# Optimization experiments

Measured on AMD Instinct MI355X. Metric: run time of the kernel, lower is better.

## Reference

```python
import jax, jax.numpy as jnp
import numpy as np

SOFTMAX_TEMP = 0.01
WINDOW_SIZE = 2
B_TOTAL, C, N = 8, 256, 512
H = W = 256


def _l2_normalize(x, axis):
    # F.normalize: x / max(||x||, eps)
    n = jnp.sqrt(jnp.sum(x * x, axis=axis, keepdims=True))
    return x / jnp.maximum(n, 1e-12)


def _bilinear_sample(img, coords):
    """Bilinear sample img [b,c,H,W] at pixel coords [b,n,2] (u=x, v=y),
    align_corners=True semantics (coords are direct pixel positions)."""
    b, c, h, w = img.shape
    u = jnp.clip(coords[..., 0], 0.0, w - 1.0)
    v = jnp.clip(coords[..., 1], 0.0, h - 1.0)
    u0 = jnp.floor(u); v0 = jnp.floor(v)
    u1 = jnp.minimum(u0 + 1.0, w - 1.0)
    v1 = jnp.minimum(v0 + 1.0, h - 1.0)
    wu = u - u0; wv = v - v0
    flat = img.reshape(b, c, h * w)
    n = coords.shape[1]
    def gather(vi, ui):
        idx = (vi * w + ui).astype(jnp.int32)  # [b,n]
        return jnp.take_along_axis(flat, jnp.broadcast_to(idx[:, None, :], (b, c, n)), axis=2)
    out = (gather(v0, u0) * ((1 - wv) * (1 - wu))[:, None, :]
           + gather(v0, u1) * ((1 - wv) * wu)[:, None, :]
           + gather(v1, u0) * (wv * (1 - wu))[:, None, :]
           + gather(v1, u1) * (wv * wu)[:, None, :])
    return out  # [b,c,n]


def setup_inputs() -> dict:
    key = jax.random.key(0)
    k1, k2, k3, k4 = jax.random.split(key, 4)
    return {
        "keypoint_scores": jax.random.uniform(k1, (B_TOTAL, 1, N), dtype=jnp.float32),
        "keypoint_desc": jax.random.normal(k2, (B_TOTAL, C, N), dtype=jnp.float32),
        "scores_dense": jax.random.uniform(k3, (B_TOTAL, 1, H, W), dtype=jnp.float32),
        "desc_dense": jax.random.normal(k4, (B_TOTAL, C, H, W), dtype=jnp.float32),
    }


def reference(keypoint_scores, keypoint_desc, scores_dense, desc_dense):
    bsz, c, n = keypoint_desc.shape
    _, _, h, w = desc_dense.shape
    bq = bsz // WINDOW_SIZE

    # src descriptors (every window_size-th frame), L2-normalized over channels
    src_desc = _l2_normalize(keypoint_desc[::WINDOW_SIZE], axis=1)          # [bq,C,N]
    # tgt dense descriptors, normalized over channels
    tgt_desc = _l2_normalize(desc_dense[1::WINDOW_SIZE].reshape(bq, c, h * w), axis=1)  # [bq,C,HW]

    # dense cosine correlation + softmax over HW
    match_vals = jnp.einsum('bcn,bcm->bnm', src_desc, tgt_desc)             # [bq,N,HW]
    soft = jax.nn.softmax(match_vals / SOFTMAX_TEMP, axis=2)

    # coordinate grid: u = x (fast, width), v = y (slow, height)
    vv, uu = jnp.meshgrid(jnp.arange(h, dtype=jnp.float32),
                          jnp.arange(w, dtype=jnp.float32), indexing='ij')
    coords = jnp.stack([uu.reshape(-1), vv.reshape(-1)], axis=1)            # [HW,2]

    # soft-argmax coordinate expectation
    pseudo_coords = jnp.einsum('bnm,mt->bnt', soft, coords)                 # [bq,N,2]

    # bilinear gathers at pseudo coords
    tgt_scores = scores_dense[1::WINDOW_SIZE]                               # [bq,1,H,W]
    pseudo_scores = _bilinear_sample(tgt_scores, pseudo_coords)             # [bq,1,N]
    pseudo_desc = _bilinear_sample(tgt_desc.reshape(bq, c, h, w), pseudo_coords)  # [bq,C,N]

    desc_match_score = jnp.sum(src_desc * pseudo_desc, axis=1, keepdims=True) / float(c)
    src_scores = keypoint_scores[::WINDOW_SIZE]                             # [bq,1,N]
    match_weights = 0.5 * (desc_match_score + 1.0) * src_scores * pseudo_scores
    return pseudo_coords, match_weights
```

## Files before the change

### kernel.cpp

```cpp
#include <hip/hip_runtime.h>
#include <math.h>

#define BQ 4
#define CC 256
#define NN 512
#define HWD 65536
#define WW 256

typedef __attribute__((ext_vector_type(8))) _Float16 f16x8;
typedef __attribute__((ext_vector_type(4))) float f32x4;

#define OB_INVT 0u
#define OB_INVS 1048576u
#define OB_PART 1056768u
#define OB_AH   2097152u
#define OB_BH   4194304u
#define WS_REQ  138412032ull

#define GLDS16(g, l) __builtin_amdgcn_global_load_lds( \
    (const __attribute__((address_space(1))) void*)(g), \
    (__attribute__((address_space(3))) void*)(l), 16, 0, 0)

__device__ inline unsigned pk2h(float x0, float x1) {
    _Float16 h0 = (_Float16)x0, h1 = (_Float16)x1;
    unsigned short u0 = __builtin_bit_cast(unsigned short, h0);
    unsigned short u1 = __builtin_bit_cast(unsigned short, h1);
    return (unsigned)u0 | ((unsigned)u1 << 16);
}

__global__ __launch_bounds__(256) void k_prep16(
    const float* __restrict__ src, size_t batch_stride, int ld, int rows_tot,
    _Float16* __restrict__ outH, float* __restrict__ invout) {
    __shared__ float raw[CC * 64];
    __shared__ float sinv[64];
    int b = blockIdx.y;
    int mb = blockIdx.x * 64;
    int tid = threadIdx.x;
    const float* S = src + (size_t)b * batch_stride;
    #pragma unroll
    for (int it = 0; it < 16; ++it) {
        int c = it * 16 + (tid >> 4);
        int m4 = (tid & 15) * 4;
        float4 v = *reinterpret_cast<const float4*>(S + (size_t)c * ld + mb + m4);
        *reinterpret_cast<float4*>(&raw[c * 64 + (m4 ^ (c & 60))]) = v;
    }
    __syncthreads();
    {
        int m = tid >> 2, part = tid & 3;
        float acc = 0.f;
        for (int i = 0; i < 64; ++i) {
            int c = part * 64 + i;
            float x = raw[c * 64 + (m ^ (c & 60))];
            acc = fmaf(x, x, acc);
        }
        acc += __shfl_xor(acc, 1);
        acc += __shfl_xor(acc, 2);
        if (part == 0) {
            float iv = 1.0f / fmaxf(sqrtf(acc), 1e-12f);
            sinv[m] = iv;
            invout[(size_t)b * rows_tot + mb + m] = iv;
        }
    }
    __syncthreads();
    int m = tid & 63, sub = tid >> 6;
    float iv = sinv[m];
    for (int kc = 0; kc < 8; ++kc) {
        int c0 = kc * 32 + sub * 8;
        unsigned hh[4];
        #pragma unroll
        for (int jp = 0; jp < 4; ++jp) {
            int c = c0 + jp * 2;
            int c1 = c + 1;
            float x0 = raw[c * 64 + (m ^ (c & 60))] * iv;
            float x1 = raw[c1 * 64 + (m ^ (c1 & 60))] * iv;
            hh[jp] = pk2h(x0, x1);
        }
        size_t base = ((size_t)(b * 8 + kc) * rows_tot + mb + m) * 32 + sub * 8;
        *reinterpret_cast<uint4*>(outH + base) = make_uint4(hh[0], hh[1], hh[2], hh[3]);
    }
}

__global__ __launch_bounds__(512, 2) void k_main3(
    const _Float16* __restrict__ Ah, const _Float16* __restrict__ Bh,
    float* __restrict__ part) {
    __shared__ __align__(16) char smem[65536];

    int p = blockIdx.x;
    int xcd = p & 7, slot = p >> 3;
    int g = slot >> 2, nt = slot & 3;
    int pair = xcd * 8 + g;
    int bb = pair >> 4, chunk = pair & 15;
    int nbase = nt * 128;

    int tid = threadIdx.x;
    int w = tid >> 6, lane = tid & 63;
    int wn = w >> 2, wm = w & 3;
    int lrow = lane & 15, lkh = lane >> 4;
    int key = (lrow >> 1) & 3;

    int sA = tid * 16;
    int rA = sA >> 6, slA = (sA >> 4) & 3;
    int seA = (rA << 5) + ((slA ^ ((rA >> 1) & 3)) << 3);
    int wb = w * 1024;

    int aoff = ((wn * 64 + lrow) << 5) + ((lkh ^ key) << 3);
    int boffG = ((wm * 64 + lrow) << 5) + (lkh << 3);

    #pragma unroll
    for (int kc = 0; kc < 8; ++kc) {
        size_t aB = ((size_t)(bb * 8 + kc) * 512 + nbase) * 32;
        GLDS16(Ah + aB + seA, smem + kc * 8192 + wb);
    }
    f16x8 breg[4][4];
    #define BLOAD(buf, ms, kc) do {                                             \
        size_t bB = ((size_t)(bb * 8 + (kc)) * 65536 + (size_t)chunk * 4096     \
                     + (size_t)(ms) * 256) * 32 + boffG;                        \
        const _Float16* bp = Bh + bB;                                           \
        breg[buf][0] = *reinterpret_cast<const f16x8*>(bp);                     \
        breg[buf][1] = *reinterpret_cast<const f16x8*>(bp + 512);               \
        breg[buf][2] = *reinterpret_cast<const f16x8*>(bp + 1024);              \
        breg[buf][3] = *reinterpret_cast<const f16x8*>(bp + 1536);              \
    } while (0)
    BLOAD(0, 0, 0);
    BLOAD(1, 0, 1);
    asm volatile("s_waitcnt vmcnt(0)" ::: "memory");
    __syncthreads();

    float s_[4][4], su_[4][4], sv_[4][4];
    #pragma unroll
    for (int i = 0; i < 4; ++i)
        #pragma unroll
        for (int j = 0; j < 4; ++j) { s_[i][j] = 0.f; su_[i][j] = 0.f; sv_[i][j] = 0.f; }

    for (int ms = 0; ms < 16; ++ms) {
        f32x4 acc[4][4];
        #pragma unroll
        for (int i = 0; i < 4; ++i)
            #pragma unroll
            for (int j = 0; j < 4; ++j) acc[i][j] = (f32x4){0.f, 0.f, 0.f, 0.f};

        #pragma unroll
        for (int kc = 0; kc < 8; ++kc) {
            int nkc = kc + 2;
            int nms = ms + (nkc >> 3);
            nkc &= 7;
            if (nms < 16) {
                BLOAD((kc + 2) & 3, nms, nkc);
                asm volatile("s_waitcnt vmcnt(8)" ::: "memory");
            } else if (kc == 6) {
                asm volatile("s_waitcnt vmcnt(4)" ::: "memory");
            } else {
                asm volatile("s_waitcnt vmcnt(0)" ::: "memory");
            }

            const _Float16* base = (const _Float16*)(smem + kc * 8192);
            f16x8 ah[4];
            #pragma unroll
            for (int rt = 0; rt < 4; ++rt)
                ah[rt] = *reinterpret_cast<const f16x8*>(base + aoff + rt * 512);

            __builtin_amdgcn_s_setprio(1);
            #pragma unroll
            for (int rt = 0; rt < 4; ++rt)
                #pragma unroll
                for (int ct = 0; ct < 4; ++ct)
                    acc[rt][ct] = __builtin_amdgcn_mfma_f32_16x16x32_f16(
                        ah[rt], breg[kc & 3][ct], acc[rt][ct], 0, 0, 0);
            __builtin_amdgcn_s_setprio(0);
        }

        float vstep = (float)(chunk * 16 + ms);
        #pragma unroll
        for (int rt = 0; rt < 4; ++rt) {
            #pragma unroll
            for (int reg = 0; reg < 4; ++reg) {
                float ts = 0.f, tu = 0.f;
                #pragma unroll
                for (int ct = 0; ct < 4; ++ct) {
                    float L = acc[rt][ct][reg];
                    float pz = __expf(fmaf(L, 100.f, -100.f));
                    ts += pz;
                    tu = fmaf(pz, (float)(wm * 64 + ct * 16 + lrow), tu);
                }
                s_[rt][reg] += ts;
                su_[rt][reg] += tu;
                sv_[rt][reg] = fmaf(vstep, ts, sv_[rt][reg]);
            }
        }
    }
    #undef BLOAD

    __syncthreads();
    float* lred = (float*)smem;
    #pragma unroll
    for (int rt = 0; rt < 4; ++rt) {
        #pragma unroll
        for (int reg = 0; reg < 4; ++reg) {
            float a = s_[rt][reg], b2 = su_[rt][reg], c2 = sv_[rt][reg];
            #pragma unroll
            for (int o = 1; o < 16; o <<= 1) {
                a += __shfl_xor(a, o);
                b2 += __shfl_xor(b2, o);
                c2 += __shfl_xor(c2, o);
            }
            if (lrow == 0) {
                int nl = rt * 16 + lkh * 4 + reg;
                lred[(w * 64 + nl) * 3 + 0] = a;
                lred[(w * 64 + nl) * 3 + 1] = b2;
                lred[(w * 64 + nl) * 3 + 2] = c2;
            }
        }
    }
    __syncthreads();
    if (tid < 128) {
        int wnl = tid >> 6, nl = tid & 63;
        float a = 0.f, b2 = 0.f, c2 = 0.f;
        #pragma unroll
        for (int q = 0; q < 4; ++q) {
            const float* p2 = &lred[((wnl * 4 + q) * 64 + nl) * 3];
            a += p2[0]; b2 += p2[1]; c2 += p2[2];
        }
        int n = nbase + wnl * 64 + nl;
        float* dst = part + ((size_t)(bb * 512 + n) * 16 + chunk) * 3;
        dst[0] = a; dst[1] = b2; dst[2] = c2;
    }
}

__global__ void k_finish2(const float* __restrict__ kscores,
                          const float* __restrict__ kdesc,
                          const float* __restrict__ sdense,
                          const float* __restrict__ desc,
                          const float* __restrict__ wsf,
                          float* __restrict__ out) {
    int bn = blockIdx.x;
    int b = bn >> 9, n = bn & 511;
    int tid = threadIdx.x;
    __shared__ float swf[8];
    __shared__ int sidx[4];
    __shared__ float red[4];

    if (tid == 0) {
        const float* pp = wsf + (OB_PART / 4) + (size_t)bn * 48;
        float S = 0.f, SU = 0.f, SV = 0.f;
        for (int k = 0; k < 16; ++k) {
            S += pp[k * 3]; SU += pp[k * 3 + 1]; SV += pp[k * 3 + 2];
        }
        float u = SU / S, v = SV / S;
        out[bn * 2 + 0] = u;
        out[bn * 2 + 1] = v;

        float uc = fminf(fmaxf(u, 0.f), 255.f);
        float vc = fminf(fmaxf(v, 0.f), 255.f);
        float u0 = floorf(uc), v0 = floorf(vc);
        float u1 = fminf(u0 + 1.f, 255.f), v1 = fminf(v0 + 1.f, 255.f);
        float wu = uc - u0, wv = vc - v0;
        int i00 = (int)v0 * WW + (int)u0;
        int i01 = (int)v0 * WW + (int)u1;
        int i10 = (int)v1 * WW + (int)u0;
        int i11 = (int)v1 * WW + (int)u1;
        float w00 = (1.f - wv) * (1.f - wu), w01 = (1.f - wv) * wu;
        float w10 = wv * (1.f - wu),         w11 = wv * wu;

        const float* sd = sdense + (size_t)(2 * b + 1) * HWD;
        float ps = w00 * sd[i00] + w01 * sd[i01] + w10 * sd[i10] + w11 * sd[i11];

        const float* it = wsf + (size_t)b * HWD;
        swf[0] = w00 * it[i00]; swf[1] = w01 * it[i01];
        swf[2] = w10 * it[i10]; swf[3] = w11 * it[i11];
        swf[4] = ps;
        sidx[0] = i00; sidx[1] = i01; sidx[2] = i10; sidx[3] = i11;
    }
    __syncthreads();

    int c = tid;
    const float* dcol = desc + (size_t)(2 * b + 1) * CC * HWD + (size_t)c * HWD;
    float pd = swf[0] * dcol[sidx[0]] + swf[1] * dcol[sidx[1]]
             + swf[2] * dcol[sidx[2]] + swf[3] * dcol[sidx[3]];
    float sc = kdesc[(size_t)(2 * b) * CC * NN + (size_t)c * NN + n];
    float t = pd * sc;
    #pragma unroll
    for (int o = 32; o > 0; o >>= 1) t += __shfl_xor(t, o);
    if ((tid & 63) == 0) red[tid >> 6] = t;
    __syncthreads();
    if (tid == 0) {
        float dot = red[0] + red[1] + red[2] + red[3];
        float invs = wsf[OB_INVS / 4 + b * 512 + n];
        float dms = dot * invs * (1.0f / 256.0f);
        float wgt = 0.5f * (dms + 1.0f) * kscores[(size_t)(2 * b) * NN + n] * swf[4];
        out[BQ * NN * 2 + bn] = wgt;
    }
}

#define MCHUNKS 16
#define MLEN (HWD / MCHUNKS)
#define TN 64
#define TM 256
#define CK 16
#define WS_INVT 0
#define WS_INVS (BQ * HWD)
#define WS_PART (WS_INVS + BQ * NN)

__global__ void fb_invt(const float* __restrict__ desc, float* __restrict__ ws) {
    int gid = blockIdx.x * blockDim.x + threadIdx.x;
    int b = gid >> 14;
    int m4 = (gid & 16383) << 2;
    const float* base = desc + (size_t)(2 * b + 1) * CC * HWD + m4;
    float ax = 0.f, ay = 0.f, az = 0.f, aw = 0.f;
    #pragma unroll 4
    for (int c = 0; c < CC; ++c) {
        float4 v = *reinterpret_cast<const float4*>(base + (size_t)c * HWD);
        ax = fmaf(v.x, v.x, ax); ay = fmaf(v.y, v.y, ay);
        az = fmaf(v.z, v.z, az); aw = fmaf(v.w, v.w, aw);
    }
    float4 r;
    r.x = 1.0f / fmaxf(sqrtf(ax), 1e-12f);
    r.y = 1.0f / fmaxf(sqrtf(ay), 1e-12f);
    r.z = 1.0f / fmaxf(sqrtf(az), 1e-12f);
    r.w = 1.0f / fmaxf(sqrtf(aw), 1e-12f);
    *reinterpret_cast<float4*>(ws + WS_INVT + b * HWD + m4) = r;
}

__global__ void fb_invs(const float* __restrict__ kdesc, float* __restrict__ ws) {
    int gid = blockIdx.x * blockDim.x + threadIdx.x;
    int b = gid >> 9;
    int n = gid & 511;
    const float* base = kdesc + (size_t)(2 * b) * CC * NN + n;
    float acc = 0.f;
    for (int c = 0; c < CC; ++c) {
        float v = base[(size_t)c * NN];
        acc = fmaf(v, v, acc);
    }
    ws[WS_INVS + b * NN + n] = 1.0f / fmaxf(sqrtf(acc), 1e-12f);
}

__global__ __launch_bounds__(256) void fb_main(
    const float* __restrict__ kdesc, const float* __restrict__ desc,
    const float* __restrict__ ws, float* __restrict__ part) {
    __shared__ float As[CK][TN];
    __shared__ float Bs[CK][TM];
    int chunk = blockIdx.x, ntile = blockIdx.y, b = blockIdx.z;
    int tid = threadIdx.x;
    int tn = tid >> 5, tm = tid & 31;
    int nbase = ntile * TN;
    const float* Ag = kdesc + (size_t)(2 * b) * CC * NN + nbase;
    const float* Bg = desc + (size_t)(2 * b + 1) * CC * HWD + (size_t)chunk * MLEN;
    const float* invt = ws + WS_INVT + (size_t)b * HWD + (size_t)chunk * MLEN;
    float sA[8];
    #pragma unroll
    for (int r = 0; r < 8; ++r)
        sA[r] = ws[WS_INVS + b * NN + nbase + tn * 8 + r] * 100.0f;
    float mx[8], s[8], su[8], sv[8];
    #pragma unroll
    for (int r = 0; r < 8; ++r) { mx[r] = -1e30f; s[r] = 0.f; su[r] = 0.f; sv[r] = 0.f; }
    for (int mt = 0; mt < MLEN; mt += TM) {
        float acc[8][8];
        #pragma unroll
        for (int r = 0; r < 8; ++r)
            #pragma unroll
            for (int j = 0; j < 8; ++j) acc[r][j] = 0.f;
        for (int c0 = 0; c0 < CC; c0 += CK) {
            int ca = tid >> 4, na = (tid & 15) << 2;
            float4 va = *reinterpret_cast<const float4*>(Ag + (size_t)(c0 + ca) * NN + na);
            int cb = tid >> 6, mb = (tid & 63) << 2;
            float4 vb[4];
            #pragma unroll
            for (int i = 0; i < 4; ++i)
                vb[i] = *reinterpret_cast<const float4*>(Bg + (size_t)(c0 + cb + 4 * i) * HWD + mt + mb);
            __syncthreads();
            *reinterpret_cast<float4*>(&As[ca][na]) = va;
            #pragma unroll
            for (int i = 0; i < 4; ++i)
                *reinterpret_cast<float4*>(&Bs[cb + 4 * i][mb]) = vb[i];
            __syncthreads();
            #pragma unroll
            for (int cc = 0; cc < CK; ++cc) {
                float a[8], bv[8];
                *reinterpret_cast<float4*>(&a[0]) = *reinterpret_cast<const float4*>(&As[cc][tn * 8]);
                *reinterpret_cast<float4*>(&a[4]) = *reinterpret_cast<const float4*>(&As[cc][tn * 8 + 4]);
                *reinterpret_cast<float4*>(&bv[0]) = *reinterpret_cast<const float4*>(&Bs[cc][tm * 8]);
                *reinterpret_cast<float4*>(&bv[4]) = *reinterpret_cast<const float4*>(&Bs[cc][tm * 8 + 4]);
                #pragma unroll
                for (int r = 0; r < 8; ++r)
                    #pragma unroll
                    for (int j = 0; j < 8; ++j)
                        acc[r][j] = fmaf(a[r], bv[j], acc[r][j]);
            }
        }
        float it[8];
        *reinterpret_cast<float4*>(&it[0]) = *reinterpret_cast<const float4*>(invt + mt + tm * 8);
        *reinterpret_cast<float4*>(&it[4]) = *reinterpret_cast<const float4*>(invt + mt + tm * 8 + 4);
        int mg0 = chunk * MLEN + mt + tm * 8;
        float vt = (float)(mg0 >> 8);
        float ub = (float)(tm * 8);
        #pragma unroll
        for (int r = 0; r < 8; ++r) {
            float L[8];
            #pragma unroll
            for (int j = 0; j < 8; ++j) L[j] = acc[r][j] * (sA[r] * it[j]);
            float tmax = L[0];
            #pragma unroll
            for (int j = 1; j < 8; ++j) tmax = fmaxf(tmax, L[j]);
            #pragma unroll
            for (int o = 1; o < 32; o <<= 1) tmax = fmaxf(tmax, __shfl_xor(tmax, o));
            float newm = fmaxf(mx[r], tmax);
            float ts = 0.f, tu = 0.f;
            #pragma unroll
            for (int j = 0; j < 8; ++j) {
                float pz = __expf(L[j] - newm);
                ts += pz;
                tu = fmaf(pz, ub + (float)j, tu);
            }
            #pragma unroll
            for (int o = 1; o < 32; o <<= 1) {
                ts += __shfl_xor(ts, o);
                tu += __shfl_xor(tu, o);
            }
            float f = __expf(mx[r] - newm);
            s[r]  = fmaf(s[r], f, ts);
            su[r] = fmaf(su[r], f, tu);
            sv[r] = fmaf(sv[r], f, vt * ts);
            mx[r] = newm;
        }
    }
    if (tm == 0) {
        #pragma unroll
        for (int r = 0; r < 8; ++r) {
            int n = nbase + tn * 8 + r;
            float4 o4 = make_float4(mx[r], s[r], su[r], sv[r]);
            *reinterpret_cast<float4*>(part + ((size_t)(b * NN + n) * MCHUNKS + chunk) * 4) = o4;
        }
    }
}

__global__ void fb_finish(const float* __restrict__ kscores,
                          const float* __restrict__ kdesc,
                          const float* __restrict__ sdense,
                          const float* __restrict__ desc,
                          const float* __restrict__ ws,
                          float* __restrict__ out) {
    int bn = blockIdx.x;
    int b = bn >> 9, n = bn & 511;
    int tid = threadIdx.x;
    __shared__ float swf[8];
    __shared__ int sidx[4];
    __shared__ float red[4];
    if (tid == 0) {
        const float* pp = ws + WS_PART + (size_t)bn * MCHUNKS * 4;
        float M = -1e30f;
        for (int k = 0; k < MCHUNKS; ++k) M = fmaxf(M, pp[4 * k]);
        float S = 0.f, SU = 0.f, SV = 0.f;
        for (int k = 0; k < MCHUNKS; ++k) {
            float f = __expf(pp[4 * k] - M);
            S  = fmaf(pp[4 * k + 1], f, S);
            SU = fmaf(pp[4 * k + 2], f, SU);
            SV = fmaf(pp[4 * k + 3], f, SV);
        }
        float u = SU / S, v = SV / S;
        out[bn * 2 + 0] = u;
        out[bn * 2 + 1] = v;
        float uc = fminf(fmaxf(u, 0.f), 255.f);
        float vc = fminf(fmaxf(v, 0.f), 255.f);
        float u0 = floorf(uc), v0 = floorf(vc);
        float u1 = fminf(u0 + 1.f, 255.f), v1 = fminf(v0 + 1.f, 255.f);
        float wu = uc - u0, wv = vc - v0;
        int i00 = (int)v0 * WW + (int)u0;
        int i01 = (int)v0 * WW + (int)u1;
        int i10 = (int)v1 * WW + (int)u0;
        int i11 = (int)v1 * WW + (int)u1;
        float w00 = (1.f - wv) * (1.f - wu), w01 = (1.f - wv) * wu;
        float w10 = wv * (1.f - wu),         w11 = wv * wu;
        const float* sd = sdense + (size_t)(2 * b + 1) * HWD;
        float ps = w00 * sd[i00] + w01 * sd[i01] + w10 * sd[i10] + w11 * sd[i11];
        const float* it = ws + WS_INVT + (size_t)b * HWD;
        swf[0] = w00 * it[i00]; swf[1] = w01 * it[i01];
        swf[2] = w10 * it[i10]; swf[3] = w11 * it[i11];
        swf[4] = ps;
        sidx[0] = i00; sidx[1] = i01; sidx[2] = i10; sidx[3] = i11;
    }
    __syncthreads();
    int c = tid;
    const float* dcol = desc + (size_t)(2 * b + 1) * CC * HWD + (size_t)c * HWD;
    float pd = swf[0] * dcol[sidx[0]] + swf[1] * dcol[sidx[1]]
             + swf[2] * dcol[sidx[2]] + swf[3] * dcol[sidx[3]];
    float sc = kdesc[(size_t)(2 * b) * CC * NN + (size_t)c * NN + n];
    float t = pd * sc;
    #pragma unroll
    for (int o = 32; o > 0; o >>= 1) t += __shfl_xor(t, o);
    if ((tid & 63) == 0) red[tid >> 6] = t;
    __syncthreads();
    if (tid == 0) {
        float dot = red[0] + red[1] + red[2] + red[3];
        float invs = ws[WS_INVS + b * NN + n];
        float dms = dot * invs * (1.0f / 256.0f);
        float wgt = 0.5f * (dms + 1.0f) * kscores[(size_t)(2 * b) * NN + n] * swf[4];
        out[BQ * NN * 2 + bn] = wgt;
    }
}

extern "C" void kernel_launch(void* const* d_in, const int* in_sizes, int n_in,
                              void* d_out, int out_size, void* d_ws, size_t ws_size,
                              hipStream_t stream) {
    const float* kscores = (const float*)d_in[0];
    const float* kdesc   = (const float*)d_in[1];
    const float* sdense  = (const float*)d_in[2];
    const float* desc    = (const float*)d_in[3];
    float* out = (float*)d_out;
    char* wsb = (char*)d_ws;
    float* wsf = (float*)d_ws;

    if (ws_size >= WS_REQ) {
        _Float16* AH = (_Float16*)(wsb + OB_AH);
        _Float16* BH = (_Float16*)(wsb + OB_BH);
        float* part = (float*)(wsb + OB_PART);

        hipLaunchKernelGGL(k_prep16, dim3(HWD / 64, BQ), dim3(256), 0, stream,
                           desc + (size_t)CC * HWD, (size_t)2 * CC * HWD, HWD, HWD,
                           BH, wsf + (OB_INVT / 4));
        hipLaunchKernelGGL(k_prep16, dim3(NN / 64, BQ), dim3(256), 0, stream,
                           kdesc, (size_t)2 * CC * NN, NN, NN,
                           AH, wsf + (OB_INVS / 4));
        hipLaunchKernelGGL(k_main3, dim3(256), dim3(512), 0, stream,
                           AH, BH, part);
        hipLaunchKernelGGL(k_finish2, dim3(BQ * NN), dim3(256), 0, stream,
                           kscores, kdesc, sdense, desc, wsf, out);
    } else {
        float* ws = wsf;
        hipLaunchKernelGGL(fb_invt, dim3(BQ * HWD / 4 / 256), dim3(256), 0, stream, desc, ws);
        hipLaunchKernelGGL(fb_invs, dim3(BQ * NN / 256), dim3(256), 0, stream, kdesc, ws);
        hipLaunchKernelGGL(fb_main, dim3(MCHUNKS, NN / TN, BQ), dim3(256), 0, stream,
                           kdesc, desc, ws, ws + WS_PART);
        hipLaunchKernelGGL(fb_finish, dim3(BQ * NN), dim3(256), 0, stream,
                           kscores, kdesc, sdense, desc, ws, out);
    }
}
```

Before: 197.2 us.

## Merge prep launches, finish from fp16 normalized buffers, hoist LDS A loads

The two normalization/fp16-conversion launches become one grid, with block index selecting the dense or keypoint source, and the inverse-norm outputs are no longer written. The finish kernel now gathers the bilinear descriptor from the already-normalized fp16 BH and AH buffers instead of strided fp32 reads from the raw dense tensor, which cuts gather traffic and launch overhead. The main GEMM loop issues its A-fragment LDS reads before the wait on the global-to-LDS prefetch to overlap latency. The finish dot product now runs in fp16-rounded precision, which changes numerics slightly.

```diff
diff --git a/kernel.cpp b/kernel.cpp
--- a/kernel.cpp
+++ b/kernel.cpp
@@ -10,8 +10,6 @@
 typedef __attribute__((ext_vector_type(8))) _Float16 f16x8;
 typedef __attribute__((ext_vector_type(4))) float f32x4;
 
-#define OB_INVT 0u
-#define OB_INVS 1048576u
 #define OB_PART 1056768u
 #define OB_AH   2097152u
 #define OB_BH   4194304u
@@ -29,14 +27,25 @@
 }
 
 __global__ __launch_bounds__(256) void k_prep16(
-    const float* __restrict__ src, size_t batch_stride, int ld, int rows_tot,
-    _Float16* __restrict__ outH, float* __restrict__ invout) {
+    const float* __restrict__ descB, const float* __restrict__ descA,
+    _Float16* __restrict__ outB, _Float16* __restrict__ outA) {
     __shared__ float raw[CC * 64];
     __shared__ float sinv[64];
     int b = blockIdx.y;
-    int mb = blockIdx.x * 64;
+    int bx = blockIdx.x;
     int tid = threadIdx.x;
-    const float* S = src + (size_t)b * batch_stride;
+
+    const float* S;
+    _Float16* outH;
+    int ld, rows_tot, mb;
+    if (bx < 1024) {
+        S = descB + (size_t)(2 * b + 1) * CC * HWD;
+        outH = outB; ld = HWD; rows_tot = HWD; mb = bx * 64;
+    } else {
+        S = descA + (size_t)(2 * b) * CC * NN;
+        outH = outA; ld = NN; rows_tot = NN; mb = (bx - 1024) * 64;
+    }
+
     #pragma unroll
     for (int it = 0; it < 16; ++it) {
         int c = it * 16 + (tid >> 4);
@@ -55,11 +64,7 @@
         }
         acc += __shfl_xor(acc, 1);
         acc += __shfl_xor(acc, 2);
-        if (part == 0) {
-            float iv = 1.0f / fmaxf(sqrtf(acc), 1e-12f);
-            sinv[m] = iv;
-            invout[(size_t)b * rows_tot + mb + m] = iv;
-        }
+        if (part == 0) sinv[m] = 1.0f / fmaxf(sqrtf(acc), 1e-12f);
     }
     __syncthreads();
     int m = tid & 63, sub = tid >> 6;
@@ -141,6 +146,12 @@
 
         #pragma unroll
         for (int kc = 0; kc < 8; ++kc) {
+            const _Float16* base = (const _Float16*)(smem + kc * 8192);
+            f16x8 ah[4];
+            #pragma unroll
+            for (int rt = 0; rt < 4; ++rt)
+                ah[rt] = *reinterpret_cast<const f16x8*>(base + aoff + rt * 512);
+
             int nkc = kc + 2;
             int nms = ms + (nkc >> 3);
             nkc &= 7;
@@ -152,12 +163,6 @@
             } else {
                 asm volatile("s_waitcnt vmcnt(0)" ::: "memory");
             }
-
-            const _Float16* base = (const _Float16*)(smem + kc * 8192);
-            f16x8 ah[4];
-            #pragma unroll
-            for (int rt = 0; rt < 4; ++rt)
-                ah[rt] = *reinterpret_cast<const f16x8*>(base + aoff + rt * 512);
 
             __builtin_amdgcn_s_setprio(1);
             #pragma unroll
@@ -226,21 +231,20 @@
     }
 }
 
-__global__ void k_finish2(const float* __restrict__ kscores,
-                          const float* __restrict__ kdesc,
-                          const float* __restrict__ sdense,
-                          const float* __restrict__ desc,
-                          const float* __restrict__ wsf,
-                          float* __restrict__ out) {
+__global__ __launch_bounds__(256) void k_finish3(
+    const float* __restrict__ kscores, const float* __restrict__ sdense,
+    const _Float16* __restrict__ AH, const _Float16* __restrict__ BH,
+    const float* __restrict__ part, float* __restrict__ out) {
     int bn = blockIdx.x;
     int b = bn >> 9, n = bn & 511;
     int tid = threadIdx.x;
-    __shared__ float swf[8];
-    __shared__ int sidx[4];
+    __shared__ float sw[4];
+    __shared__ int sm[4];
+    __shared__ float sps;
     __shared__ float red[4];
 
     if (tid == 0) {
-        const float* pp = wsf + (OB_PART / 4) + (size_t)bn * 48;
+        const float* pp = part + (size_t)bn * 48;
         float S = 0.f, SU = 0.f, SV = 0.f;
         for (int k = 0; k < 16; ++k) {
             S += pp[k * 3]; SU += pp[k * 3 + 1]; SV += pp[k * 3 + 2];
@@ -258,35 +262,32 @@
         int i01 = (int)v0 * WW + (int)u1;
         int i10 = (int)v1 * WW + (int)u0;
         int i11 = (int)v1 * WW + (int)u1;
-        float w00 = (1.f - wv) * (1.f - wu), w01 = (1.f - wv) * wu;
-        float w10 = wv * (1.f - wu),         w11 = wv * wu;
+        sw[0] = (1.f - wv) * (1.f - wu); sw[1] = (1.f - wv) * wu;
+        sw[2] = wv * (1.f - wu);         sw[3] = wv * wu;
+        sm[0] = i00; sm[1] = i01; sm[2] = i10; sm[3] = i11;
 
         const float* sd = sdense + (size_t)(2 * b + 1) * HWD;
-        float ps = w00 * sd[i00] + w01 * sd[i01] + w10 * sd[i10] + w11 * sd[i11];
-
-        const float* it = wsf + (size_t)b * HWD;
-        swf[0] = w00 * it[i00]; swf[1] = w01 * it[i01];
-        swf[2] = w10 * it[i10]; swf[3] = w11 * it[i11];
-        swf[4] = ps;
-        sidx[0] = i00; sidx[1] = i01; sidx[2] = i10; sidx[3] = i11;
-    }
-    __syncthreads();
-
-    int c = tid;
-    const float* dcol = desc + (size_t)(2 * b + 1) * CC * HWD + (size_t)c * HWD;
-    float pd = swf[0] * dcol[sidx[0]] + swf[1] * dcol[sidx[1]]
-             + swf[2] * dcol[sidx[2]] + swf[3] * dcol[sidx[3]];
-    float sc = kdesc[(size_t)(2 * b) * CC * NN + (size_t)c * NN + n];
-    float t = pd * sc;
-    #pragma unroll
-    for (int o = 32; o > 0; o >>= 1) t += __shfl_xor(t, o);
+        sps = sw[0] * sd[i00] + sw[1] * sd[i01] + sw[2] * sd[i10] + sw[3] * sd[i11];
+    }
+    __syncthreads();
+
+    int kc = tid >> 5, e = tid & 31;
+    float a = (float)AH[((size_t)(b * 8 + kc) * 512 + n) * 32 + e];
+    float pdc = 0.f;
+    #pragma unroll
+    for (int wq = 0; wq < 4; ++wq) {
+        float bv = (float)BH[((size_t)(b * 8 + kc) * 65536 + sm[wq]) * 32 + e];
+        pdc = fmaf(sw[wq], bv, pdc);
+    }
+    float t = a * pdc;
+    #pragma unroll
+    for (int o = 1; o < 64; o <<= 1) t += __shfl_xor(t, o);
     if ((tid & 63) == 0) red[tid >> 6] = t;
     __syncthreads();
     if (tid == 0) {
         float dot = red[0] + red[1] + red[2] + red[3];
-        float invs = wsf[OB_INVS / 4 + b * 512 + n];
-        float dms = dot * invs * (1.0f / 256.0f);
-        float wgt = 0.5f * (dms + 1.0f) * kscores[(size_t)(2 * b) * NN + n] * swf[4];
+        float dms = dot * (1.0f / 256.0f);
+        float wgt = 0.5f * (dms + 1.0f) * kscores[(size_t)(2 * b) * NN + n] * sps;
         out[BQ * NN * 2 + bn] = wgt;
     }
 }
@@ -513,16 +514,12 @@
         _Float16* BH = (_Float16*)(wsb + OB_BH);
         float* part = (float*)(wsb + OB_PART);
 
-        hipLaunchKernelGGL(k_prep16, dim3(HWD / 64, BQ), dim3(256), 0, stream,
-                           desc + (size_t)CC * HWD, (size_t)2 * CC * HWD, HWD, HWD,
-                           BH, wsf + (OB_INVT / 4));
-        hipLaunchKernelGGL(k_prep16, dim3(NN / 64, BQ), dim3(256), 0, stream,
-                           kdesc, (size_t)2 * CC * NN, NN, NN,
-                           AH, wsf + (OB_INVS / 4));
+        hipLaunchKernelGGL(k_prep16, dim3(1024 + NN / 64, BQ), dim3(256), 0, stream,
+                           desc, kdesc, BH, AH);
         hipLaunchKernelGGL(k_main3, dim3(256), dim3(512), 0, stream,
                            AH, BH, part);
-        hipLaunchKernelGGL(k_finish2, dim3(BQ * NN), dim3(256), 0, stream,
-                           kscores, kdesc, sdense, desc, wsf, out);
+        hipLaunchKernelGGL(k_finish3, dim3(BQ * NN), dim3(256), 0, stream,
+                           kscores, sdense, AH, BH, part, out);
     } else {
         float* ws = wsf;
         hipLaunchKernelGGL(fb_invt, dim3(BQ * HWD / 4 / 256), dim3(256), 0, stream, desc, ws);
```

Measured after the change: 173.4 us (median of 2 runs). 1.14x faster.
